# Kernel tuning notes

Measured on AMD Instinct MI355X. Metric: run time of the kernel, lower is better.

Reference implementation:

```python
import jax, jax.numpy as jnp
import numpy as np

N, E = 4096, 4096          # nodes, hyperedges
IN_DIM, OUT_DIM, EDGE_DIM = 256, 256, 64
HEADS, DEG, CARD = 8, 8, 8  # node degree, edge cardinality (regular hypergraph)


def setup_inputs() -> dict:
    key = jax.random.key(0)
    ks = jax.random.split(key, 6)
    # regular hypergraph: DEG rounds, each a permutation of nodes chunked into
    # blocks of CARD -> every node in exactly DEG edges, every edge has CARD
    # distinct nodes. E = DEG * N / CARD.
    rng = np.random.default_rng(0)
    node_of_edge = np.concatenate(
        [rng.permutation(N).reshape(-1, CARD) for _ in range(DEG)], axis=0)  # [E, CARD]
    inc = np.zeros((E, N), dtype=np.float32)
    inc[np.arange(E)[:, None], node_of_edge] = 1.0
    s = 0.05
    return {
        "x": jax.random.normal(ks[0], (N, IN_DIM), jnp.float32),
        "incidence": jnp.asarray(inc),
        "edge_attr": jax.random.normal(ks[1], (E, EDGE_DIM), jnp.float32),
        "W_lin": jax.random.normal(ks[2], (IN_DIM, OUT_DIM), jnp.float32) * s,
        "W_edge": jax.random.normal(ks[3], (EDGE_DIM, OUT_DIM), jnp.float32) * s,
        "in_proj_w": jax.random.normal(ks[4], (3 * OUT_DIM, OUT_DIM), jnp.float32) * s,
        "in_proj_b": jnp.zeros((3 * OUT_DIM,), jnp.float32),
        "out_proj_w": jax.random.normal(ks[5], (OUT_DIM, OUT_DIM), jnp.float32) * s,
        "out_proj_b": jnp.zeros((OUT_DIM,), jnp.float32),
        "deg": DEG,
        "card": CARD,
    }


def reference(x, incidence, edge_attr, W_lin, W_edge,
              in_proj_w, in_proj_b, out_proj_w, out_proj_b, deg, card):
    n = x.shape[0]
    Wh = x @ W_lin          # [N, D]
    We = edge_attr @ W_edge  # [E, D]
    Dm = Wh.shape[1]
    H = HEADS
    dh = Dm // H
    # recover regular structure from the binary incidence matrix.
    # (attention is permutation-invariant over the pair set, so the order of
    #  indices returned by top_k vs torch.nonzero does not matter)
    _, edge_of_node = jax.lax.top_k(incidence.T, deg)   # [N, deg]
    _, node_of_edge = jax.lax.top_k(incidence, card)    # [E, card]
    pair_e = edge_of_node[:, :, None]                   # [N, deg, 1]
    pair_u = node_of_edge[edge_of_node]                 # [N, deg, card]
    L = deg * card
    Ksrc = (Wh[pair_u] + We[pair_e]).reshape(n, L, Dm)  # key source per pair
    Vsrc = Wh[pair_u].reshape(n, L, Dm)                 # value source per pair
    # torch nn.MultiheadAttention in/out projections
    Wq, Wk, Wv = jnp.split(in_proj_w, 3, axis=0)
    bq, bk, bv = jnp.split(in_proj_b, 3)
    q = (Wh @ Wq.T + bq).reshape(n, H, dh)              # q_len = 1 per node
    k = (Ksrc @ Wk.T + bk).reshape(n, L, H, dh)
    v = (Vsrc @ Wv.T + bv).reshape(n, L, H, dh)
    scale = 1.0 / jnp.sqrt(jnp.asarray(dh, q.dtype))
    scores = jnp.einsum('nhd,nlhd->nhl', q, k) * scale  # [N, H, L]
    attn = jax.nn.softmax(scores, axis=-1)
    ctx = jnp.einsum('nhl,nlhd->nhd', attn, v).reshape(n, Dm)
    out = ctx @ out_proj_w.T + out_proj_b
    return jax.nn.relu(out)
```

## Files before the change

### kernel.cpp

```cpp
#include <hip/hip_runtime.h>
#include <hip/hip_bf16.h>

#define NN    4096
#define EE    4096
#define DM    256
#define EDIM  64
#define HH    8
#define DHd   32
#define LL    64

typedef short  s16x8 __attribute__((ext_vector_type(8)));
typedef unsigned short u16x8 __attribute__((ext_vector_type(8)));
typedef float  f32x4 __attribute__((ext_vector_type(4)));
typedef unsigned int u32x4v __attribute__((ext_vector_type(4)));

#define SCALE 0.17677669529663687f

__device__ __forceinline__ float b2f(unsigned short u) {
  return __uint_as_float(((unsigned int)u) << 16);
}
__device__ __forceinline__ unsigned short f2b_bits(float f) {
  unsigned int u = __float_as_uint(f);
  u = (u + 0x7FFFu + ((u >> 16) & 1u)) >> 16;
  return (unsigned short)u;
}

#if __has_builtin(__builtin_amdgcn_fdot2_f32_bf16)
#define HAVE_DOT2B 1
typedef __bf16 bf2v __attribute__((ext_vector_type(2)));
__device__ __forceinline__ float dot2b(unsigned int a, unsigned int b, float c) {
  return __builtin_amdgcn_fdot2_f32_bf16(__builtin_bit_cast(bf2v, a),
                                         __builtin_bit_cast(bf2v, b), c, false);
}
#else
#define HAVE_DOT2B 0
#endif

#if __has_builtin(__builtin_amdgcn_update_dpp) && __has_builtin(__builtin_amdgcn_readfirstlane)
#define HAVE_DPP 1
template <int CTRL>
__device__ __forceinline__ float dpp_sum_step(float x) {
  int s = __builtin_amdgcn_update_dpp(0, __float_as_int(x), CTRL, 0xF, 0xF, true);
  return x + __int_as_float(s);
}
#else
#define HAVE_DPP 0
#endif

#define MODE_PLAIN 0
#define MODE_PROJ  1
#define MODE_OUT   2

__device__ __forceinline__ void gemm_mfma_body(
    short* As, short* Bs, f32x4 acc[2][2], int wr, int wc, int fr, int fk) {
  s16x8 af0 = *(const s16x8*)&As[(wr + fr) * 40 + fk];
  s16x8 af1 = *(const s16x8*)&As[(wr + 16 + fr) * 40 + fk];
  s16x8 bf0 = *(const s16x8*)&Bs[(wc + fr) * 40 + fk];
  s16x8 bf1 = *(const s16x8*)&Bs[(wc + 16 + fr) * 40 + fk];
  acc[0][0] = __builtin_amdgcn_mfma_f32_16x16x32_bf16(af0, bf0, acc[0][0], 0, 0, 0);
  acc[0][1] = __builtin_amdgcn_mfma_f32_16x16x32_bf16(af0, bf1, acc[0][1], 0, 0, 0);
  acc[1][0] = __builtin_amdgcn_mfma_f32_16x16x32_bf16(af1, bf0, acc[1][0], 0, 0, 0);
  acc[1][1] = __builtin_amdgcn_mfma_f32_16x16x32_bf16(af1, bf1, acc[1][1], 0, 0, 0);
}

__device__ __forceinline__ void gemm_tile(
    const unsigned short* __restrict__ A, const unsigned short* __restrict__ B,
    int i0, int j0, int N, int K, int mode,
    float* __restrict__ out_f, unsigned short* __restrict__ out_b,
    unsigned short* __restrict__ out_b2, const float* __restrict__ bias,
    short* As, short* Bs) {
  const int tid  = threadIdx.x;
  const int wid  = tid >> 6, lane = tid & 63;
  const int wr   = (wid >> 1) * 32, wc = (wid & 1) * 32;
  const int srow = tid >> 2, schunk = (tid & 3) * 8;
  const int fr   = lane & 15, fk = (lane >> 4) * 8;

  f32x4 acc[2][2];
#pragma unroll
  for (int a = 0; a < 2; ++a)
#pragma unroll
    for (int b = 0; b < 2; ++b) acc[a][b] = (f32x4){0.f, 0.f, 0.f, 0.f};

  for (int kk = 0; kk < K; kk += 32) {
    *(s16x8*)&As[srow * 40 + schunk] = *(const s16x8*)&A[(size_t)(i0 + srow) * K + kk + schunk];
    *(s16x8*)&Bs[srow * 40 + schunk] = *(const s16x8*)&B[(size_t)(j0 + srow) * K + kk + schunk];
    __syncthreads();
    gemm_mfma_body(As, Bs, acc, wr, wc, fr, fk);
    __syncthreads();
  }

  const int ecol = lane & 15, erow0 = (lane >> 4) * 4;
#pragma unroll
  for (int mi = 0; mi < 2; ++mi)
#pragma unroll
    for (int ni = 0; ni < 2; ++ni) {
#pragma unroll
      for (int v = 0; v < 4; ++v) {
        int i = i0 + wr + mi * 16 + erow0 + v;
        int j = j0 + wc + ni * 16 + ecol;
        float val = acc[mi][ni][v];
        if (mode == MODE_PLAIN) {
          out_b[(size_t)i * N + j] = f2b_bits(val);
        } else if (mode == MODE_PROJ) {
          if (j < 256)      out_b[(size_t)i * 256 + j]           = f2b_bits((val + bias[j]) * SCALE);
          else if (j < 512) out_b2[(size_t)i * 256 + (j - 256)]  = f2b_bits(val);
          else              ((unsigned short*)out_f)[(size_t)i * 256 + (j - 512)] = f2b_bits(val + bias[j]);
        } else {
          float r = val + bias[j];
          out_f[(size_t)i * N + j] = r > 0.f ? r : 0.f;
        }
      }
    }
}

__device__ __forceinline__ void gemm_tile_f32src(
    const float* __restrict__ A, const float* __restrict__ B,
    int i0, int j0, int N, int K,
    unsigned short* __restrict__ out_b, short* As, short* Bs) {
  const int tid  = threadIdx.x;
  const int wid  = tid >> 6, lane = tid & 63;
  const int wr   = (wid >> 1) * 32, wc = (wid & 1) * 32;
  const int srow = tid >> 2, schunk = (tid & 3) * 8;
  const int fr   = lane & 15, fk = (lane >> 4) * 8;

  f32x4 acc[2][2];
#pragma unroll
  for (int a = 0; a < 2; ++a)
#pragma unroll
    for (int b = 0; b < 2; ++b) acc[a][b] = (f32x4){0.f, 0.f, 0.f, 0.f};

  for (int kk = 0; kk < K; kk += 32) {
    float4 a0 = *(const float4*)&A[(size_t)(i0 + srow) * K + kk + schunk];
    float4 a1 = *(const float4*)&A[(size_t)(i0 + srow) * K + kk + schunk + 4];
    float4 b0 = *(const float4*)&B[(size_t)(j0 + srow) * K + kk + schunk];
    float4 b1 = *(const float4*)&B[(size_t)(j0 + srow) * K + kk + schunk + 4];
    s16x8 av, bv;
    av[0] = (short)f2b_bits(a0.x); av[1] = (short)f2b_bits(a0.y);
    av[2] = (short)f2b_bits(a0.z); av[3] = (short)f2b_bits(a0.w);
    av[4] = (short)f2b_bits(a1.x); av[5] = (short)f2b_bits(a1.y);
    av[6] = (short)f2b_bits(a1.z); av[7] = (short)f2b_bits(a1.w);
    bv[0] = (short)f2b_bits(b0.x); bv[1] = (short)f2b_bits(b0.y);
    bv[2] = (short)f2b_bits(b0.z); bv[3] = (short)f2b_bits(b0.w);
    bv[4] = (short)f2b_bits(b1.x); bv[5] = (short)f2b_bits(b1.y);
    bv[6] = (short)f2b_bits(b1.z); bv[7] = (short)f2b_bits(b1.w);
    *(s16x8*)&As[srow * 40 + schunk] = av;
    *(s16x8*)&Bs[srow * 40 + schunk] = bv;
    __syncthreads();
    gemm_mfma_body(As, Bs, acc, wr, wc, fr, fk);
    __syncthreads();
  }

  const int ecol = lane & 15, erow0 = (lane >> 4) * 4;
#pragma unroll
  for (int mi = 0; mi < 2; ++mi)
#pragma unroll
    for (int ni = 0; ni < 2; ++ni)
#pragma unroll
      for (int v = 0; v < 4; ++v) {
        int i = i0 + wr + mi * 16 + erow0 + v;
        int j = j0 + wc + ni * 16 + ecol;
        if (j < N) out_b[(size_t)i * N + j] = f2b_bits(acc[mi][ni][v]);
      }
}

__global__ __launch_bounds__(256) void mega1(
    const float* __restrict__ inc,
    int* __restrict__ cnt_e, int* __restrict__ cnt_n,
    int* __restrict__ noe, int* __restrict__ eon,
    const float* __restrict__ x, const float* __restrict__ ea,
    const float* __restrict__ wout,
    unsigned short* __restrict__ xb, unsigned short* __restrict__ eab,
    unsigned short* __restrict__ woutb,
    const float* __restrict__ ipw, const float* __restrict__ wlin,
    const float* __restrict__ wedge,
    unsigned short* __restrict__ F, unsigned short* __restrict__ G) {
  __shared__ short As[64 * 40] __attribute__((aligned(16)));
  __shared__ short Bs[64 * 40] __attribute__((aligned(16)));
  const int bid = blockIdx.x;
  if (bid < 16384) {
    int t = bid * 256 + threadIdx.x;
    float4 v = ((const float4*)inc)[t];
    int flat = t * 4;
    int e  = flat >> 12;
    int u0 = flat & 4095;
    float vals[4] = {v.x, v.y, v.z, v.w};
#pragma unroll
    for (int j = 0; j < 4; ++j) {
      if (vals[j] != 0.0f) {
        int u  = u0 + j;
        int pe = atomicAdd(&cnt_e[e], 1);
        noe[e * 8 + pe] = u;
        int pn = atomicAdd(&cnt_n[u], 1);
        eon[u * 8 + pn] = e;
      }
    }
    return;
  }
  if (bid < 17728) {
    int j = (bid - 16384) * 256 + threadIdx.x;
    const float* src; unsigned short* dst;
    if (j < 262144)      { src = x;    dst = xb; }
    else { j -= 262144;
    if (j < 65536)       { src = ea;   dst = eab; }
    else { j -= 65536;     src = wout; dst = woutb; } }
    float4 v = ((const float4*)src)[j];
    ushort4 o;
    o.x = f2b_bits(v.x); o.y = f2b_bits(v.y); o.z = f2b_bits(v.z); o.w = f2b_bits(v.w);
    ((ushort4*)dst)[j] = o;
    return;
  }
  int fb = bid - 17728;
  if (fb < 48) {
    gemm_tile_f32src(ipw, wlin, (fb >> 2) * 64, (fb & 3) * 64, 256, 256, F, As, Bs);
  } else {
    gemm_tile_f32src(ipw + 65536, wedge, (fb - 48) * 64, 0, 64, 256, G, As, Bs);
  }
}

__global__ __launch_bounds__(256) void mega2(
    const unsigned short* __restrict__ x_bf, const unsigned short* __restrict__ F,
    const unsigned short* __restrict__ ea_bf, const unsigned short* __restrict__ G,
    unsigned short* __restrict__ Q, unsigned short* __restrict__ Kn,
    unsigned short* __restrict__ Vn, unsigned short* __restrict__ Ke,
    const float* __restrict__ ipb,
    const int* __restrict__ eon, const int* __restrict__ noe,
    int* __restrict__ pair_u) {
  __shared__ short As[64 * 40] __attribute__((aligned(16)));
  __shared__ short Bs[64 * 40] __attribute__((aligned(16)));
  const int bid = blockIdx.x;
  if (bid < 768) {
    gemm_tile(x_bf, F, (bid & 63) * 64, (bid >> 6) * 64, 768, 256,
              MODE_PROJ, (float*)Vn, Q, Kn, ipb, As, Bs);
  } else if (bid < 1024) {
    int r = bid - 768;
    gemm_tile(ea_bf, G, (r & 63) * 64, (r >> 6) * 64, 256, 64,
              MODE_PLAIN, nullptr, Ke, nullptr, nullptr, As, Bs);
  } else {
    int wv = ((bid - 1024) * 256 + threadIdx.x) >> 6;
    int lane = threadIdx.x & 63;
#pragma unroll
    for (int r = 0; r < 16; ++r) {
      int n = wv * 16 + r;
      int e = eon[n * 8 + (lane >> 3)];
      pair_u[n * 64 + lane] = noe[e * 8 + (lane & 7)];
    }
  }
}

__global__ __launch_bounds__(512) void attn_kernel(
    const unsigned short* __restrict__ Q, const unsigned short* __restrict__ Kn,
    const unsigned short* __restrict__ Vn, const unsigned short* __restrict__ Ke,
    const int* __restrict__ eon, const int* __restrict__ pair_u,
    unsigned short* __restrict__ ctx) {
  const int n = blockIdx.x;
  __shared__ unsigned short Klds[64 * 256] __attribute__((aligned(16)));
  __shared__ unsigned short Elds[8 * 256]  __attribute__((aligned(16)));
  __shared__ float Alds[8 * 64];
  const int tid = threadIdx.x;
  const int h = tid >> 6, lane = tid & 63;
  const int rg = lane & 15, dchunk = lane >> 4;

#pragma unroll
  for (int j = 0; j < 4; ++j) {
    int row = h * 8 + j * 2 + (lane >> 5);
    int u   = pair_u[n * 64 + row];
    u16x8 v = *(const u16x8*)(Kn + (size_t)u * 256 + (lane & 31) * 8);
    int db  = (row * 512 + (lane & 31) * 16) ^ ((row & 7) << 4);
    *(u16x8*)((char*)Klds + db) = v;
  }
  {
    int e = eon[n * 8 + h];
    if (lane < 32) {
      u16x8 v = *(const u16x8*)(Ke + (size_t)e * 256 + lane * 8);
      int db  = (h * 512 + lane * 16) ^ ((h & 7) << 4);
      *(u16x8*)((char*)Elds + db) = v;
    }
  }

  u16x8 vstage[4];
#pragma unroll
  for (int i = 0; i < 4; ++i) {
    int u = pair_u[n * 64 + rg * 4 + i];
    vstage[i] = *(const u16x8*)(Vn + (size_t)u * 256 + h * 32 + dchunk * 8);
  }
  u16x8 qstage[4];
  {
    const u16x8* qp = (const u16x8*)(Q + (size_t)n * 256 + h * 32);
#pragma unroll
    for (int c = 0; c < 4; ++c) qstage[c] = qp[c];
  }

  __syncthreads();

  const int kbase = lane * 512 + h * 64, ksw = (lane & 7) << 4;
  const int ebase = (lane >> 3) * 512 + h * 64, esw = ((lane >> 3) & 7) << 4;
  float s;
  {
    float s1 = 0.f, s2 = 0.f;
#pragma unroll
    for (int c = 0; c < 4; ++c) {
      u16x8 kv = *(const u16x8*)((const char*)Klds + ((kbase + c * 16) ^ ksw));
      u16x8 ev = *(const u16x8*)((const char*)Elds + ((ebase + c * 16) ^ esw));
      u16x8 qv = qstage[c];
#if HAVE_DOT2B
      u32x4v kw = __builtin_bit_cast(u32x4v, kv);
      u32x4v ew = __builtin_bit_cast(u32x4v, ev);
      u32x4v qw = __builtin_bit_cast(u32x4v, qv);
#pragma unroll
      for (int p = 0; p < 4; ++p) {
        s1 = dot2b(qw[p], kw[p], s1);
        s2 = dot2b(qw[p], ew[p], s2);
      }
#else
#pragma unroll
      for (int j = 0; j < 8; ++j)
        s1 += b2f(qv[j]) * (b2f(kv[j]) + b2f(ev[j]));
#endif
    }
    s = s1 + s2;
  }

  float p = __expf(s - 8.0f);
  float t = p + __shfl_xor(p, 16);
  t = t + __shfl_xor(t, 32);
#if HAVE_DPP
  t = dpp_sum_step<0x101>(t);
  t = dpp_sum_step<0x102>(t);
  t = dpp_sum_step<0x104>(t);
  t = dpp_sum_step<0x108>(t);
  float sum = __uint_as_float((unsigned)__builtin_amdgcn_readfirstlane(__float_as_int(t)));
#else
  t += __shfl_xor(t, 1); t += __shfl_xor(t, 2);
  t += __shfl_xor(t, 4); t += __shfl_xor(t, 8);
  float sum = t;
#endif
  const float a = __fdividef(p, sum);

  Alds[(h << 6) | lane] = a;
  float4 aq = *(const float4*)&Alds[(h << 6) | (rg * 4)];

  float acc[8];
#pragma unroll
  for (int j = 0; j < 8; ++j) acc[j] = 0.f;
#if HAVE_DOT2B
  {
    unsigned int pw01 = (unsigned int)f2b_bits(aq.x) | ((unsigned int)f2b_bits(aq.y) << 16);
    unsigned int pw23 = (unsigned int)f2b_bits(aq.z) | ((unsigned int)f2b_bits(aq.w) << 16);
    u32x4v v0 = __builtin_bit_cast(u32x4v, vstage[0]);
    u32x4v v1 = __builtin_bit_cast(u32x4v, vstage[1]);
    u32x4v v2 = __builtin_bit_cast(u32x4v, vstage[2]);
    u32x4v v3 = __builtin_bit_cast(u32x4v, vstage[3]);
#pragma unroll
    for (int jw = 0; jw < 4; ++jw) {
      unsigned int a01 = __builtin_amdgcn_perm(v1[jw], v0[jw], 0x05040100u);
      unsigned int b01 = __builtin_amdgcn_perm(v1[jw], v0[jw], 0x07060302u);
      unsigned int a23 = __builtin_amdgcn_perm(v3[jw], v2[jw], 0x05040100u);
      unsigned int b23 = __builtin_amdgcn_perm(v3[jw], v2[jw], 0x07060302u);
      acc[jw * 2]     = dot2b(pw01, a01, acc[jw * 2]);
      acc[jw * 2]     = dot2b(pw23, a23, acc[jw * 2]);
      acc[jw * 2 + 1] = dot2b(pw01, b01, acc[jw * 2 + 1]);
      acc[jw * 2 + 1] = dot2b(pw23, b23, acc[jw * 2 + 1]);
    }
  }
#else
#pragma unroll
  for (int i = 0; i < 4; ++i) {
    float pi = (i == 0) ? aq.x : (i == 1) ? aq.y : (i == 2) ? aq.z : aq.w;
#pragma unroll
    for (int j = 0; j < 8; ++j) acc[j] += pi * b2f(vstage[i][j]);
  }
#endif

#if HAVE_DPP
#pragma unroll
  for (int j = 0; j < 8; ++j) {
    acc[j] = dpp_sum_step<0x101>(acc[j]);
    acc[j] = dpp_sum_step<0x102>(acc[j]);
    acc[j] = dpp_sum_step<0x104>(acc[j]);
    acc[j] = dpp_sum_step<0x108>(acc[j]);
  }
#else
#pragma unroll
  for (int off = 1; off < 16; off <<= 1)
#pragma unroll
    for (int j = 0; j < 8; ++j) acc[j] += __shfl_xor(acc[j], off, 64);
#endif

  if (rg == 0) {
    u16x8 o;
#pragma unroll
    for (int j = 0; j < 8; ++j) o[j] = f2b_bits(acc[j]);
    *(u16x8*)(ctx + (size_t)n * 256 + h * 32 + dchunk * 8) = o;
  }
}

__global__ __launch_bounds__(256) void gemm_out(
    const unsigned short* __restrict__ ctx, const unsigned short* __restrict__ wout_bf,
    float* __restrict__ out, const float* __restrict__ bias) {
  __shared__ short As[64 * 40] __attribute__((aligned(16)));
  __shared__ short Bs[64 * 40] __attribute__((aligned(16)));
  gemm_tile(ctx, wout_bf, blockIdx.x * 64, blockIdx.y * 64, 256, 256,
            MODE_OUT, out, nullptr, nullptr, bias, As, Bs);
}

#define MB_ ((size_t)1048576)
#define OFF_Q      ((size_t)0)
#define OFF_KN     (2*MB_)
#define OFF_VN     (4*MB_)
#define OFF_KE     (6*MB_)
#define OFF_CTX    (8*MB_)
#define OFF_XBF    (10*MB_)
#define OFF_EABF   (12*MB_)
#define OFF_WOUTBF (12*MB_+524288)
#define OFF_F      (13*MB_)
#define OFF_G      (13*MB_+524288)
#define OFF_PAIRU  (14*MB_)
#define OFF_CNTE   (15*MB_)
#define OFF_CNTN   (15*MB_+16384)
#define OFF_NOE    (15*MB_+32768)
#define OFF_EON    (15*MB_+163840)

extern "C" void kernel_launch(void* const* d_in, const int* in_sizes, int n_in,
                              void* d_out, int out_size, void* d_ws, size_t ws_size,
                              hipStream_t stream) {
  const float* x     = (const float*)d_in[0];
  const float* inc   = (const float*)d_in[1];
  const float* ea    = (const float*)d_in[2];
  const float* wlin  = (const float*)d_in[3];
  const float* wedge = (const float*)d_in[4];
  const float* ipw   = (const float*)d_in[5];
  const float* ipb   = (const float*)d_in[6];
  const float* wout  = (const float*)d_in[7];
  const float* outb  = (const float*)d_in[8];

  char* ws = (char*)d_ws;
  unsigned short* Q       = (unsigned short*)(ws + OFF_Q);
  unsigned short* Kn      = (unsigned short*)(ws + OFF_KN);
  unsigned short* Vn      = (unsigned short*)(ws + OFF_VN);
  unsigned short* Ke      = (unsigned short*)(ws + OFF_KE);
  unsigned short* ctx     = (unsigned short*)(ws + OFF_CTX);
  unsigned short* x_bf    = (unsigned short*)(ws + OFF_XBF);
  unsigned short* ea_bf   = (unsigned short*)(ws + OFF_EABF);
  unsigned short* wout_bf = (unsigned short*)(ws + OFF_WOUTBF);
  unsigned short* F       = (unsigned short*)(ws + OFF_F);
  unsigned short* G       = (unsigned short*)(ws + OFF_G);
  int*            cnt_e   = (int*)(ws + OFF_CNTE);
  int*            noe     = (int*)(ws + OFF_NOE);
  int*            eon     = (int*)(ws + OFF_EON);
  int*            pair_u  = (int*)(ws + OFF_PAIRU);

  hipMemsetAsync(ws + OFF_CNTE, 0, 32768, stream);

  mega1<<<17780, 256, 0, stream>>>(inc, cnt_e, (int*)(ws + OFF_CNTN), noe, eon,
                                   x, ea, wout, x_bf, ea_bf, wout_bf,
                                   ipw, wlin, wedge, F, G);
  mega2<<<1088, 256, 0, stream>>>(x_bf, F, ea_bf, G, Q, Kn, Vn, Ke, ipb,
                                  eon, noe, pair_u);
  attn_kernel<<<4096, 512, 0, stream>>>(Q, Kn, Vn, Ke, eon, pair_u, ctx);
  gemm_out<<<dim3(64, 4), 256, 0, stream>>>(ctx, wout_bf, (float*)d_out, outb);
}
```

Before: 81.00 us.

## Fuse all stages into one persistent cooperative kernel with grid syncs

Replaces the memset plus four separate launches with a single cooperative persistent kernel of 512 blocks. Grid-wide barriers separate the incidence scan and bf16 conversion, the projection GEMMs, attention and the output GEMM. The aim is to remove launch gaps and the memset. In exchange, each phase gets fewer blocks: the incidence scan runs on 460 blocks instead of about 16k, and attention processes two heads per wave over eight iterations. The original multi-kernel path is kept as a fallback when occupancy is insufficient or the cooperative launch fails.

```diff
diff --git a/kernel.cpp b/kernel.cpp
--- a/kernel.cpp
+++ b/kernel.cpp
@@ -1,5 +1,8 @@
 #include <hip/hip_runtime.h>
 #include <hip/hip_bf16.h>
+#include <hip/hip_cooperative_groups.h>
+
+namespace cg = cooperative_groups;
 
 #define NN    4096
 #define EE    4096
@@ -161,6 +164,285 @@
         int j = j0 + wc + ni * 16 + ecol;
         if (j < N) out_b[(size_t)i * N + j] = f2b_bits(acc[mi][ni][v]);
       }
+}
+
+__device__ __forceinline__ void attn_head_math(
+    const unsigned short* Klds, const unsigned short* Elds, float* Alds_wave,
+    const u16x8 qstage[4], const u16x8 vstage[4],
+    int h, int lane, int rg, int dchunk,
+    unsigned short* __restrict__ ctx, size_t ctx_off) {
+  const int kbase = lane * 512 + h * 64, ksw = (lane & 7) << 4;
+  const int ebase = (lane >> 3) * 512 + h * 64, esw = ((lane >> 3) & 7) << 4;
+  float s;
+  {
+    float s1 = 0.f, s2 = 0.f;
+#pragma unroll
+    for (int c = 0; c < 4; ++c) {
+      u16x8 kv = *(const u16x8*)((const char*)Klds + ((kbase + c * 16) ^ ksw));
+      u16x8 ev = *(const u16x8*)((const char*)Elds + ((ebase + c * 16) ^ esw));
+      u16x8 qv = qstage[c];
+#if HAVE_DOT2B
+      u32x4v kw = __builtin_bit_cast(u32x4v, kv);
+      u32x4v ew = __builtin_bit_cast(u32x4v, ev);
+      u32x4v qw = __builtin_bit_cast(u32x4v, qv);
+#pragma unroll
+      for (int p = 0; p < 4; ++p) {
+        s1 = dot2b(qw[p], kw[p], s1);
+        s2 = dot2b(qw[p], ew[p], s2);
+      }
+#else
+#pragma unroll
+      for (int j = 0; j < 8; ++j)
+        s1 += b2f(qv[j]) * (b2f(kv[j]) + b2f(ev[j]));
+#endif
+    }
+    s = s1 + s2;
+  }
+  float p = __expf(s - 8.0f);
+  float t = p + __shfl_xor(p, 16);
+  t = t + __shfl_xor(t, 32);
+#if HAVE_DPP
+  t = dpp_sum_step<0x101>(t);
+  t = dpp_sum_step<0x102>(t);
+  t = dpp_sum_step<0x104>(t);
+  t = dpp_sum_step<0x108>(t);
+  float sum = __uint_as_float((unsigned)__builtin_amdgcn_readfirstlane(__float_as_int(t)));
+#else
+  t += __shfl_xor(t, 1); t += __shfl_xor(t, 2);
+  t += __shfl_xor(t, 4); t += __shfl_xor(t, 8);
+  float sum = t;
+#endif
+  const float a = __fdividef(p, sum);
+
+  Alds_wave[lane] = a;
+  float4 aq = *(const float4*)&Alds_wave[rg * 4];
+
+  float acc[8];
+#pragma unroll
+  for (int j = 0; j < 8; ++j) acc[j] = 0.f;
+#if HAVE_DOT2B
+  {
+    unsigned int pw01 = (unsigned int)f2b_bits(aq.x) | ((unsigned int)f2b_bits(aq.y) << 16);
+    unsigned int pw23 = (unsigned int)f2b_bits(aq.z) | ((unsigned int)f2b_bits(aq.w) << 16);
+    u32x4v v0 = __builtin_bit_cast(u32x4v, vstage[0]);
+    u32x4v v1 = __builtin_bit_cast(u32x4v, vstage[1]);
+    u32x4v v2 = __builtin_bit_cast(u32x4v, vstage[2]);
+    u32x4v v3 = __builtin_bit_cast(u32x4v, vstage[3]);
+#pragma unroll
+    for (int jw = 0; jw < 4; ++jw) {
+      unsigned int a01 = __builtin_amdgcn_perm(v1[jw], v0[jw], 0x05040100u);
+      unsigned int b01 = __builtin_amdgcn_perm(v1[jw], v0[jw], 0x07060302u);
+      unsigned int a23 = __builtin_amdgcn_perm(v3[jw], v2[jw], 0x05040100u);
+      unsigned int b23 = __builtin_amdgcn_perm(v3[jw], v2[jw], 0x07060302u);
+      acc[jw * 2]     = dot2b(pw01, a01, acc[jw * 2]);
+      acc[jw * 2]     = dot2b(pw23, a23, acc[jw * 2]);
+      acc[jw * 2 + 1] = dot2b(pw01, b01, acc[jw * 2 + 1]);
+      acc[jw * 2 + 1] = dot2b(pw23, b23, acc[jw * 2 + 1]);
+    }
+  }
+#else
+#pragma unroll
+  for (int i = 0; i < 4; ++i) {
+    float pi = (i == 0) ? aq.x : (i == 1) ? aq.y : (i == 2) ? aq.z : aq.w;
+#pragma unroll
+    for (int j = 0; j < 8; ++j) acc[j] += pi * b2f(vstage[i][j]);
+  }
+#endif
+#if HAVE_DPP
+#pragma unroll
+  for (int j = 0; j < 8; ++j) {
+    acc[j] = dpp_sum_step<0x101>(acc[j]);
+    acc[j] = dpp_sum_step<0x102>(acc[j]);
+    acc[j] = dpp_sum_step<0x104>(acc[j]);
+    acc[j] = dpp_sum_step<0x108>(acc[j]);
+  }
+#else
+#pragma unroll
+  for (int off = 1; off < 16; off <<= 1)
+#pragma unroll
+    for (int j = 0; j < 8; ++j) acc[j] += __shfl_xor(acc[j], off, 64);
+#endif
+  if (rg == 0) {
+    u16x8 o;
+#pragma unroll
+    for (int j = 0; j < 8; ++j) o[j] = f2b_bits(acc[j]);
+    *(u16x8*)(ctx + ctx_off + h * 32 + dchunk * 8) = o;
+  }
+}
+
+#define MB_ ((size_t)1048576)
+#define OFF_Q      ((size_t)0)
+#define OFF_KN     (2*MB_)
+#define OFF_VN     (4*MB_)
+#define OFF_KE     (6*MB_)
+#define OFF_CTX    (8*MB_)
+#define OFF_XBF    (10*MB_)
+#define OFF_EABF   (12*MB_)
+#define OFF_WOUTBF (12*MB_+524288)
+#define OFF_F      (13*MB_)
+#define OFF_G      (13*MB_+524288)
+#define OFF_PAIRU  (14*MB_)
+#define OFF_CNTE   (15*MB_)
+#define OFF_NOE    (15*MB_+32768)
+#define OFF_EON    (15*MB_+163840)
+
+__global__ __launch_bounds__(256, 2) void fused_all(
+    const float* __restrict__ inc, const float* __restrict__ x,
+    const float* __restrict__ ea, const float* __restrict__ wlin,
+    const float* __restrict__ wedge, const float* __restrict__ ipw,
+    const float* __restrict__ ipb, const float* __restrict__ wout,
+    const float* __restrict__ outb, char* __restrict__ ws,
+    float* __restrict__ out) {
+  cg::grid_group grid = cg::this_grid();
+  __shared__ char smem[37888] __attribute__((aligned(16)));
+  short* As = (short*)smem;
+  short* Bs = (short*)(smem + 5120);
+
+  unsigned short* Q       = (unsigned short*)(ws + OFF_Q);
+  unsigned short* Kn      = (unsigned short*)(ws + OFF_KN);
+  unsigned short* Vn      = (unsigned short*)(ws + OFF_VN);
+  unsigned short* Ke      = (unsigned short*)(ws + OFF_KE);
+  unsigned short* ctx     = (unsigned short*)(ws + OFF_CTX);
+  unsigned short* x_bf    = (unsigned short*)(ws + OFF_XBF);
+  unsigned short* ea_bf   = (unsigned short*)(ws + OFF_EABF);
+  unsigned short* wout_bf = (unsigned short*)(ws + OFF_WOUTBF);
+  unsigned short* F       = (unsigned short*)(ws + OFF_F);
+  unsigned short* G       = (unsigned short*)(ws + OFF_G);
+  int*            cnt     = (int*)(ws + OFF_CNTE);
+  int*            noe     = (int*)(ws + OFF_NOE);
+  int*            eon     = (int*)(ws + OFF_EON);
+  int*            pair_u  = (int*)(ws + OFF_PAIRU);
+
+  const int bid = blockIdx.x, tid = threadIdx.x;
+  const int gtid = bid * 256 + tid;
+
+  if (gtid < 8192) cnt[gtid] = 0;
+  __threadfence();
+  grid.sync();
+  __threadfence();
+
+  if (bid < 52) {
+    if (bid < 48) {
+      gemm_tile_f32src(ipw, wlin, (bid >> 2) * 64, (bid & 3) * 64, 256, 256, F, As, Bs);
+    } else {
+      gemm_tile_f32src(ipw + 65536, wedge, (bid - 48) * 64, 0, 64, 256, G, As, Bs);
+    }
+  } else {
+    int* cnt_e = cnt;
+    int* cnt_n = cnt + 4096;
+    for (int i = (bid - 52) * 256 + tid; i < 4194304; i += 460 * 256) {
+      float4 v = ((const float4*)inc)[i];
+      int flat = i * 4;
+      int e  = flat >> 12;
+      int u0 = flat & 4095;
+      float vals[4] = {v.x, v.y, v.z, v.w};
+#pragma unroll
+      for (int j = 0; j < 4; ++j) {
+        if (vals[j] != 0.0f) {
+          int u  = u0 + j;
+          int pe = atomicAdd(&cnt_e[e], 1);
+          noe[e * 8 + pe] = u;
+          int pn = atomicAdd(&cnt_n[u], 1);
+          eon[u * 8 + pn] = e;
+        }
+      }
+    }
+    for (int i = (bid - 52) * 256 + tid; i < 344064; i += 460 * 256) {
+      const float* src; unsigned short* dst; int j = i;
+      if (j < 262144)      { src = x;    dst = x_bf; }
+      else { j -= 262144;
+      if (j < 65536)       { src = ea;   dst = ea_bf; }
+      else { j -= 65536;     src = wout; dst = wout_bf; } }
+      float4 v = ((const float4*)src)[j];
+      ushort4 o;
+      o.x = f2b_bits(v.x); o.y = f2b_bits(v.y); o.z = f2b_bits(v.z); o.w = f2b_bits(v.w);
+      ((ushort4*)dst)[j] = o;
+    }
+  }
+  __threadfence();
+  grid.sync();
+  __threadfence();
+
+#pragma unroll
+  for (int uu = 0; uu < 2; ++uu) {
+    int unit = bid + uu * 512;
+    if (unit < 768) {
+      gemm_tile(x_bf, F, (unit & 63) * 64, (unit >> 6) * 64, 768, 256,
+                MODE_PROJ, (float*)Vn, Q, Kn, ipb, As, Bs);
+    } else {
+      int r = unit - 768;
+      gemm_tile(ea_bf, G, (r & 63) * 64, (r >> 6) * 64, 256, 64,
+                MODE_PLAIN, nullptr, Ke, nullptr, nullptr, As, Bs);
+    }
+  }
+  if (bid < 64) {
+    int gw = bid * 4 + (tid >> 6);
+    int lane = tid & 63;
+#pragma unroll
+    for (int rr = 0; rr < 16; ++rr) {
+      int n = gw * 16 + rr;
+      int e = eon[n * 8 + (lane >> 3)];
+      pair_u[n * 64 + lane] = noe[e * 8 + (lane & 7)];
+    }
+  }
+  __threadfence();
+  grid.sync();
+  __threadfence();
+
+  {
+    unsigned short* Klds = (unsigned short*)smem;
+    unsigned short* Elds = (unsigned short*)(smem + 32768);
+    float*          Alds = (float*)(smem + 36864);
+    const int wid = tid >> 6, lane = tid & 63;
+    const int rg = lane & 15, dchunk = lane >> 4;
+
+    for (int it = 0; it < 8; ++it) {
+      const int n = it * 512 + bid;
+      __syncthreads();
+#pragma unroll
+      for (int j = 0; j < 8; ++j) {
+        int row = wid * 16 + j * 2 + (lane >> 5);
+        int u   = pair_u[n * 64 + row];
+        u16x8 v = *(const u16x8*)(Kn + (size_t)u * 256 + (lane & 31) * 8);
+        int db  = (row * 512 + (lane & 31) * 16) ^ ((row & 7) << 4);
+        *(u16x8*)((char*)Klds + db) = v;
+      }
+      {
+        int row = wid * 2 + (lane >> 5);
+        int e   = eon[n * 8 + row];
+        u16x8 v = *(const u16x8*)(Ke + (size_t)e * 256 + (lane & 31) * 8);
+        int db  = (row * 512 + (lane & 31) * 16) ^ ((row & 7) << 4);
+        *(u16x8*)((char*)Elds + db) = v;
+      }
+      u16x8 vstage[2][4], qstage[2][4];
+#pragma unroll
+      for (int hp = 0; hp < 2; ++hp) {
+        const int h = wid * 2 + hp;
+#pragma unroll
+        for (int i = 0; i < 4; ++i) {
+          int u = pair_u[n * 64 + rg * 4 + i];
+          vstage[hp][i] = *(const u16x8*)(Vn + (size_t)u * 256 + h * 32 + dchunk * 8);
+        }
+        const u16x8* qp = (const u16x8*)(Q + (size_t)n * 256 + h * 32);
+#pragma unroll
+        for (int c = 0; c < 4; ++c) qstage[hp][c] = qp[c];
+      }
+      __syncthreads();
+#pragma unroll
+      for (int hp = 0; hp < 2; ++hp) {
+        attn_head_math(Klds, Elds, &Alds[wid << 6], qstage[hp], vstage[hp],
+                       wid * 2 + hp, lane, rg, dchunk, ctx, (size_t)n * 256);
+      }
+    }
+  }
+  __threadfence();
+  grid.sync();
+  __threadfence();
+
+  if (bid < 256) {
+    gemm_tile(ctx, wout_bf, (bid & 63) * 64, (bid >> 6) * 64, 256, 256,
+              MODE_OUT, out, nullptr, nullptr, outb, As, Bs);
+  }
 }
 
 __global__ __launch_bounds__(256) void mega1(
@@ -276,7 +558,6 @@
       *(u16x8*)((char*)Elds + db) = v;
     }
   }
-
   u16x8 vstage[4];
 #pragma unroll
   for (int i = 0; i < 4; ++i) {
@@ -289,109 +570,9 @@
 #pragma unroll
     for (int c = 0; c < 4; ++c) qstage[c] = qp[c];
   }
-
   __syncthreads();
-
-  const int kbase = lane * 512 + h * 64, ksw = (lane & 7) << 4;
-  const int ebase = (lane >> 3) * 512 + h * 64, esw = ((lane >> 3) & 7) << 4;
-  float s;
-  {
-    float s1 = 0.f, s2 = 0.f;
-#pragma unroll
-    for (int c = 0; c < 4; ++c) {
-      u16x8 kv = *(const u16x8*)((const char*)Klds + ((kbase + c * 16) ^ ksw));
-      u16x8 ev = *(const u16x8*)((const char*)Elds + ((ebase + c * 16) ^ esw));
-      u16x8 qv = qstage[c];
-#if HAVE_DOT2B
-      u32x4v kw = __builtin_bit_cast(u32x4v, kv);
-      u32x4v ew = __builtin_bit_cast(u32x4v, ev);
-      u32x4v qw = __builtin_bit_cast(u32x4v, qv);
-#pragma unroll
-      for (int p = 0; p < 4; ++p) {
-        s1 = dot2b(qw[p], kw[p], s1);
-        s2 = dot2b(qw[p], ew[p], s2);
-      }
-#else
-#pragma unroll
-      for (int j = 0; j < 8; ++j)
-        s1 += b2f(qv[j]) * (b2f(kv[j]) + b2f(ev[j]));
-#endif
-    }
-    s = s1 + s2;
-  }
-
-  float p = __expf(s - 8.0f);
-  float t = p + __shfl_xor(p, 16);
-  t = t + __shfl_xor(t, 32);
-#if HAVE_DPP
-  t = dpp_sum_step<0x101>(t);
-  t = dpp_sum_step<0x102>(t);
-  t = dpp_sum_step<0x104>(t);
-  t = dpp_sum_step<0x108>(t);
-  float sum = __uint_as_float((unsigned)__builtin_amdgcn_readfirstlane(__float_as_int(t)));
-#else
-  t += __shfl_xor(t, 1); t += __shfl_xor(t, 2);
-  t += __shfl_xor(t, 4); t += __shfl_xor(t, 8);
-  float sum = t;
-#endif
-  const float a = __fdividef(p, sum);
-
-  Alds[(h << 6) | lane] = a;
-  float4 aq = *(const float4*)&Alds[(h << 6) | (rg * 4)];
-
-  float acc[8];
-#pragma unroll
-  for (int j = 0; j < 8; ++j) acc[j] = 0.f;
-#if HAVE_DOT2B
-  {
-    unsigned int pw01 = (unsigned int)f2b_bits(aq.x) | ((unsigned int)f2b_bits(aq.y) << 16);
-    unsigned int pw23 = (unsigned int)f2b_bits(aq.z) | ((unsigned int)f2b_bits(aq.w) << 16);
-    u32x4v v0 = __builtin_bit_cast(u32x4v, vstage[0]);
-    u32x4v v1 = __builtin_bit_cast(u32x4v, vstage[1]);
-    u32x4v v2 = __builtin_bit_cast(u32x4v, vstage[2]);
-    u32x4v v3 = __builtin_bit_cast(u32x4v, vstage[3]);
-#pragma unroll
-    for (int jw = 0; jw < 4; ++jw) {
-      unsigned int a01 = __builtin_amdgcn_perm(v1[jw], v0[jw], 0x05040100u);
-      unsigned int b01 = __builtin_amdgcn_perm(v1[jw], v0[jw], 0x07060302u);
-      unsigned int a23 = __builtin_amdgcn_perm(v3[jw], v2[jw], 0x05040100u);
-      unsigned int b23 = __builtin_amdgcn_perm(v3[jw], v2[jw], 0x07060302u);
-      acc[jw * 2]     = dot2b(pw01, a01, acc[jw * 2]);
-      acc[jw * 2]     = dot2b(pw23, a23, acc[jw * 2]);
-      acc[jw * 2 + 1] = dot2b(pw01, b01, acc[jw * 2 + 1]);
-      acc[jw * 2 + 1] = dot2b(pw23, b23, acc[jw * 2 + 1]);
-    }
-  }
-#else
-#pragma unroll
-  for (int i = 0; i < 4; ++i) {
-    float pi = (i == 0) ? aq.x : (i == 1) ? aq.y : (i == 2) ? aq.z : aq.w;
-#pragma unroll
-    for (int j = 0; j < 8; ++j) acc[j] += pi * b2f(vstage[i][j]);
-  }
-#endif
-
-#if HAVE_DPP
-#pragma unroll
-  for (int j = 0; j < 8; ++j) {
-    acc[j] = dpp_sum_step<0x101>(acc[j]);
-    acc[j] = dpp_sum_step<0x102>(acc[j]);
-    acc[j] = dpp_sum_step<0x104>(acc[j]);
-    acc[j] = dpp_sum_step<0x108>(acc[j]);
-  }
-#else
-#pragma unroll
-  for (int off = 1; off < 16; off <<= 1)
-#pragma unroll
-    for (int j = 0; j < 8; ++j) acc[j] += __shfl_xor(acc[j], off, 64);
-#endif
-
-  if (rg == 0) {
-    u16x8 o;
-#pragma unroll
-    for (int j = 0; j < 8; ++j) o[j] = f2b_bits(acc[j]);
-    *(u16x8*)(ctx + (size_t)n * 256 + h * 32 + dchunk * 8) = o;
-  }
+  attn_head_math(Klds, Elds, &Alds[h << 6], qstage, vstage,
+                 h, lane, rg, dchunk, ctx, (size_t)n * 256);
 }
 
 __global__ __launch_bounds__(256) void gemm_out(
@@ -402,23 +583,6 @@
   gemm_tile(ctx, wout_bf, blockIdx.x * 64, blockIdx.y * 64, 256, 256,
             MODE_OUT, out, nullptr, nullptr, bias, As, Bs);
 }
-
-#define MB_ ((size_t)1048576)
-#define OFF_Q      ((size_t)0)
-#define OFF_KN     (2*MB_)
-#define OFF_VN     (4*MB_)
-#define OFF_KE     (6*MB_)
-#define OFF_CTX    (8*MB_)
-#define OFF_XBF    (10*MB_)
-#define OFF_EABF   (12*MB_)
-#define OFF_WOUTBF (12*MB_+524288)
-#define OFF_F      (13*MB_)
-#define OFF_G      (13*MB_+524288)
-#define OFF_PAIRU  (14*MB_)
-#define OFF_CNTE   (15*MB_)
-#define OFF_CNTN   (15*MB_+16384)
-#define OFF_NOE    (15*MB_+32768)
-#define OFF_EON    (15*MB_+163840)
 
 extern "C" void kernel_launch(void* const* d_in, const int* in_sizes, int n_in,
                               void* d_out, int out_size, void* d_ws, size_t ws_size,
@@ -432,8 +596,31 @@
   const float* ipb   = (const float*)d_in[6];
   const float* wout  = (const float*)d_in[7];
   const float* outb  = (const float*)d_in[8];
-
   char* ws = (char*)d_ws;
+  float* out = (float*)d_out;
+
+  bool use_coop = false;
+  {
+    int occ = 0;
+    hipError_t e1 = hipOccupancyMaxActiveBlocksPerMultiprocessor(
+        &occ, (const void*)fused_all, 256, 0);
+    hipDeviceProp_t props;
+    hipError_t e2 = hipGetDeviceProperties(&props, 0);
+    if (e1 == hipSuccess && e2 == hipSuccess &&
+        occ >= 2 && occ * props.multiProcessorCount >= 512)
+      use_coop = true;
+  }
+
+  if (use_coop) {
+    void* args[] = {
+      (void*)&inc, (void*)&x, (void*)&ea, (void*)&wlin, (void*)&wedge,
+      (void*)&ipw, (void*)&ipb, (void*)&wout, (void*)&outb, (void*)&ws, (void*)&out
+    };
+    hipError_t e = hipLaunchCooperativeKernel((const void*)fused_all, dim3(512),
+                                              dim3(256), args, 0, stream);
+    if (e == hipSuccess) return;
+  }
+
   unsigned short* Q       = (unsigned short*)(ws + OFF_Q);
   unsigned short* Kn      = (unsigned short*)(ws + OFF_KN);
   unsigned short* Vn      = (unsigned short*)(ws + OFF_VN);
@@ -450,12 +637,11 @@
   int*            pair_u  = (int*)(ws + OFF_PAIRU);
 
   hipMemsetAsync(ws + OFF_CNTE, 0, 32768, stream);
-
-  mega1<<<17780, 256, 0, stream>>>(inc, cnt_e, (int*)(ws + OFF_CNTN), noe, eon,
+  mega1<<<17780, 256, 0, stream>>>(inc, cnt_e, (int*)(ws + OFF_CNTE) + 4096, noe, eon,
                                    x, ea, wout, x_bf, ea_bf, wout_bf,
                                    ipw, wlin, wedge, F, G);
   mega2<<<1088, 256, 0, stream>>>(x_bf, F, ea_bf, G, Q, Kn, Vn, Ke, ipb,
                                   eon, noe, pair_u);
   attn_kernel<<<4096, 512, 0, stream>>>(Q, Kn, Vn, Ke, eon, pair_u, ctx);
-  gemm_out<<<dim3(64, 4), 256, 0, stream>>>(ctx, wout_bf, (float*)d_out, outb);
-}
+  gemm_out<<<dim3(64, 4), 256, 0, stream>>>(ctx, wout_bf, out, outb);
+}
```

After: 80.17 us. No clear change (-1.0%).
